# Performance work log

Hardware: AMD Instinct MI355X
Metric: run time of the kernel (lower is better)

Reference implementation:

```python
import jax, jax.numpy as jnp
import numpy as np

B, N, S, H = 8, 512, 4096, 1024

def setup_inputs() -> dict:
    key = jax.random.key(0)
    k1, k2, k3 = jax.random.split(key, 3)
    doc_state = jax.random.normal(k1, (B, S, H), dtype=jnp.float32)
    # token->node membership mask (soft weights in [0,1), structurally a sparse/binary mask)
    nodes_mapping = jax.random.uniform(k2, (B, N, S), dtype=jnp.float32)
    # node lengths: positive, in [1, S) to avoid divide-by-near-zero
    nodes_len = jax.random.uniform(k3, (B, N), dtype=jnp.float32, minval=1.0, maxval=float(S))
    return {"doc_state": doc_state, "nodes_mapping": nodes_mapping, "nodes_len": nodes_len}

def reference(doc_state, nodes_mapping, nodes_len):
    # Faithful math: sum_s nodes_mapping[b,n,s] * doc_state[b,s,h] / nodes_len[b,n]
    # Expressed as a batched matmul instead of materializing [B,N,S,H].
    pooled = jnp.einsum('bns,bsh->bnh', nodes_mapping, doc_state)
    return pooled / nodes_len[:, :, None]
```

## Files before the change

kernel.cpp:

```cpp
#include <hip/hip_runtime.h>
#include <hip/hip_bf16.h>


typedef __bf16 bf16x8 __attribute__((ext_vector_type(8)));
typedef float  f32x4  __attribute__((ext_vector_type(4)));

#define MFMA16(a, b, c) __builtin_amdgcn_mfma_f32_16x16x32_bf16(a, b, c, 0, 0, 0)

constexpr int Bsz = 8;
constexpr int Nn  = 512;
constexpr int Ss  = 4096;
constexpr int Hh  = 1024;

constexpr int BM = 128, BN = 128, BK = 32;
constexpr int LDK = BK + 8;
constexpr int NT = Ss / BK;

__global__ __launch_bounds__(256, 1)
void mean_pool_gemm(const float* __restrict__ doc,
                    const float* __restrict__ map,
                    const float* __restrict__ len,
                    float* __restrict__ out)
{
    __shared__ __align__(16) __bf16 As[2][BM * LDK];
    __shared__ __align__(16) __bf16 Bs[2][BN * LDK];

    const int blk = blockIdx.x;
    const int b   = blk >> 5;
    const int mt  = (blk >> 3) & 3;
    const int ht  = blk & 7;
    const int n0  = mt * BM;
    const int h0  = ht * BN;

    const int tid  = threadIdx.x;
    const int wave = tid >> 6;
    const int lane = tid & 63;
    const int wr   = wave >> 1;
    const int wc   = wave & 1;
    const int l15  = lane & 15;
    const int l4   = lane >> 4;

    const float* Ab = map + (size_t)b * Nn * Ss + (size_t)n0 * Ss;
    const float* Bb = doc + (size_t)b * Ss * Hh + h0;

    const int ra = tid >> 1;
    const int ka = (tid & 1) * 16;
    const int hb  = tid & 127;
    const int kb0 = tid >> 7;

    f32x4 aR[4];
    float bR[2][8];
    f32x4 acc[4][4] = {};

    {
        const float* ap = Ab + (size_t)ra * Ss + ka;
        #pragma unroll
        for (int i = 0; i < 4; i++) aR[i] = *(const f32x4*)(ap + i * 4);
        #pragma unroll
        for (int tt = 0; tt < 2; tt++) {
            const float* bp = Bb + (size_t)((kb0 + tt * 2) * 8) * Hh + hb;
            #pragma unroll
            for (int j = 0; j < 8; j++) bR[tt][j] = bp[(size_t)j * Hh];
        }
        bf16x8 v0, v1;
        #pragma unroll
        for (int i = 0; i < 8; i++) {
            v0[i] = (__bf16)aR[i >> 2][i & 3];
            v1[i] = (__bf16)aR[2 + (i >> 2)][i & 3];
        }
        *(bf16x8*)&As[0][ra * LDK + ka]     = v0;
        *(bf16x8*)&As[0][ra * LDK + ka + 8] = v1;
        #pragma unroll
        for (int tt = 0; tt < 2; tt++) {
            bf16x8 w;
            #pragma unroll
            for (int j = 0; j < 8; j++) w[j] = (__bf16)bR[tt][j];
            *(bf16x8*)&Bs[0][hb * LDK + (kb0 + tt * 2) * 8] = w;
        }
    }
    __syncthreads();

    int cur = 0;
    for (int t = 0; t < NT; ++t) {
        if (t + 1 < NT) {
            const int s0 = (t + 1) * BK;
            const float* ap = Ab + (size_t)ra * Ss + s0 + ka;
            #pragma unroll
            for (int i = 0; i < 4; i++) aR[i] = *(const f32x4*)(ap + i * 4);
            #pragma unroll
            for (int tt = 0; tt < 2; tt++) {
                const float* bp = Bb + (size_t)(s0 + (kb0 + tt * 2) * 8) * Hh + hb;
                #pragma unroll
                for (int j = 0; j < 8; j++) bR[tt][j] = bp[(size_t)j * Hh];
            }
        }

        {
            bf16x8 aF[4], bF[4];
            #pragma unroll
            for (int m = 0; m < 4; m++)
                aF[m] = *(const bf16x8*)&As[cur][(wr * 64 + m * 16 + l15) * LDK + l4 * 8];
            #pragma unroll
            for (int n = 0; n < 4; n++)
                bF[n] = *(const bf16x8*)&Bs[cur][(wc * 64 + n * 16 + l15) * LDK + l4 * 8];
            #pragma unroll
            for (int m = 0; m < 4; m++)
                #pragma unroll
                for (int n = 0; n < 4; n++)
                    acc[m][n] = MFMA16(aF[m], bF[n], acc[m][n]);
        }

        if (t + 1 < NT) {
            __syncthreads();
            bf16x8 v0, v1;
            #pragma unroll
            for (int i = 0; i < 8; i++) {
                v0[i] = (__bf16)aR[i >> 2][i & 3];
                v1[i] = (__bf16)aR[2 + (i >> 2)][i & 3];
            }
            *(bf16x8*)&As[cur ^ 1][ra * LDK + ka]     = v0;
            *(bf16x8*)&As[cur ^ 1][ra * LDK + ka + 8] = v1;
            #pragma unroll
            for (int tt = 0; tt < 2; tt++) {
                bf16x8 w;
                #pragma unroll
                for (int j = 0; j < 8; j++) w[j] = (__bf16)bR[tt][j];
                *(bf16x8*)&Bs[cur ^ 1][hb * LDK + (kb0 + tt * 2) * 8] = w;
            }
            __syncthreads();
            cur ^= 1;
        }
    }

    const float* lenb = len + b * Nn + n0 + wr * 64;
    float* ob = out + (size_t)b * Nn * Hh + (size_t)(n0 + wr * 64) * Hh + h0 + wc * 64;
    #pragma unroll
    for (int m = 0; m < 4; m++) {
        float inv[4];
        #pragma unroll
        for (int j = 0; j < 4; j++) inv[j] = 1.0f / lenb[m * 16 + l4 * 4 + j];
        #pragma unroll
        for (int n = 0; n < 4; n++) {
            #pragma unroll
            for (int j = 0; j < 4; j++) {
                const int row = m * 16 + l4 * 4 + j;
                ob[(size_t)row * Hh + n * 16 + l15] = acc[m][n][j] * inv[j];
            }
        }
    }
}

extern "C" void kernel_launch(void* const* d_in, const int* in_sizes, int n_in,
                              void* d_out, int out_size, void* d_ws, size_t ws_size,
                              hipStream_t stream) {
    const float* doc = (const float*)d_in[0];
    const float* map = (const float*)d_in[1];
    const float* len = (const float*)d_in[2];
    float* out = (float*)d_out;

    dim3 grid(Bsz * (Nn / BM) * (Hh / BN));
    dim3 block(256);
    hipLaunchKernelGGL(mean_pool_gemm, grid, block, 0, stream, doc, map, len, out);
}
```

Measured before the change: 322.2 us.

## Shrink GEMM tiles to 64x64 and remap blocks so each batch stays on one XCD

Tiles shrink from 128x128 to 64x64, which raises the grid from 256 to 1024 workgroups and allows up to four per CU so the MI355X's compute units are fully occupied. The block index is also permuted so that consecutive hardware-dispatched blocks, which go round-robin across the 8 XCDs, map to the same batch on one XCD. This is meant to improve L2 reuse of the fp32 operands. The cost is less data reuse per tile, so each workgroup loads more global memory and issues fewer MFMAs per shared-memory load.

```diff
diff --git a/kernel.cpp b/kernel.cpp
--- a/kernel.cpp
+++ b/kernel.cpp
@@ -12,11 +12,12 @@
 constexpr int Ss  = 4096;
 constexpr int Hh  = 1024;
 
-constexpr int BM = 128, BN = 128, BK = 32;
+constexpr int BM = 64, BN = 64, BK = 32;
 constexpr int LDK = BK + 8;
 constexpr int NT = Ss / BK;
+constexpr int NWG = Bsz * (Nn / BM) * (Hh / BN);
 
-__global__ __launch_bounds__(256, 1)
+__global__ __launch_bounds__(256, 4)
 void mean_pool_gemm(const float* __restrict__ doc,
                     const float* __restrict__ map,
                     const float* __restrict__ len,
@@ -25,10 +26,12 @@
     __shared__ __align__(16) __bf16 As[2][BM * LDK];
     __shared__ __align__(16) __bf16 Bs[2][BN * LDK];
 
-    const int blk = blockIdx.x;
-    const int b   = blk >> 5;
-    const int mt  = (blk >> 3) & 3;
-    const int ht  = blk & 7;
+    const int blk = (blockIdx.x & 7) * (NWG / 8) + (blockIdx.x >> 3);
+
+    const int b   = blk >> 7;
+    const int rem = blk & 127;
+    const int mt  = rem >> 4;
+    const int ht  = rem & 15;
     const int n0  = mt * BM;
     const int h0  = ht * BN;
 
@@ -43,40 +46,31 @@
     const float* Ab = map + (size_t)b * Nn * Ss + (size_t)n0 * Ss;
     const float* Bb = doc + (size_t)b * Ss * Hh + h0;
 
-    const int ra = tid >> 1;
-    const int ka = (tid & 1) * 16;
-    const int hb  = tid & 127;
-    const int kb0 = tid >> 7;
+    const int ra = tid >> 2;
+    const int ka = (tid & 3) * 8;
+    const int hbb = tid & 63;
+    const int kb  = tid >> 6;
 
-    f32x4 aR[4];
-    float bR[2][8];
-    f32x4 acc[4][4] = {};
+    f32x4 aR[2];
+    float bR[8];
+    f32x4 acc[2][2] = {};
 
     {
         const float* ap = Ab + (size_t)ra * Ss + ka;
+        aR[0] = *(const f32x4*)(ap);
+        aR[1] = *(const f32x4*)(ap + 4);
+        const float* bp = Bb + (size_t)(kb * 8) * Hh + hbb;
         #pragma unroll
-        for (int i = 0; i < 4; i++) aR[i] = *(const f32x4*)(ap + i * 4);
-        #pragma unroll
-        for (int tt = 0; tt < 2; tt++) {
-            const float* bp = Bb + (size_t)((kb0 + tt * 2) * 8) * Hh + hb;
-            #pragma unroll
-            for (int j = 0; j < 8; j++) bR[tt][j] = bp[(size_t)j * Hh];
-        }
-        bf16x8 v0, v1;
+        for (int j = 0; j < 8; j++) bR[j] = bp[(size_t)j * Hh];
+
+        bf16x8 va, vb;
         #pragma unroll
         for (int i = 0; i < 8; i++) {
-            v0[i] = (__bf16)aR[i >> 2][i & 3];
-            v1[i] = (__bf16)aR[2 + (i >> 2)][i & 3];
+            va[i] = (__bf16)aR[i >> 2][i & 3];
+            vb[i] = (__bf16)bR[i];
         }
-        *(bf16x8*)&As[0][ra * LDK + ka]     = v0;
-        *(bf16x8*)&As[0][ra * LDK + ka + 8] = v1;
-        #pragma unroll
-        for (int tt = 0; tt < 2; tt++) {
-            bf16x8 w;
-            #pragma unroll
-            for (int j = 0; j < 8; j++) w[j] = (__bf16)bR[tt][j];
-            *(bf16x8*)&Bs[0][hb * LDK + (kb0 + tt * 2) * 8] = w;
-        }
+        *(bf16x8*)&As[0][ra * LDK + ka]      = va;
+        *(bf16x8*)&Bs[0][hbb * LDK + kb * 8] = vb;
     }
     __syncthreads();
 
@@ -85,62 +79,52 @@
         if (t + 1 < NT) {
             const int s0 = (t + 1) * BK;
             const float* ap = Ab + (size_t)ra * Ss + s0 + ka;
+            aR[0] = *(const f32x4*)(ap);
+            aR[1] = *(const f32x4*)(ap + 4);
+            const float* bp = Bb + (size_t)(s0 + kb * 8) * Hh + hbb;
             #pragma unroll
-            for (int i = 0; i < 4; i++) aR[i] = *(const f32x4*)(ap + i * 4);
-            #pragma unroll
-            for (int tt = 0; tt < 2; tt++) {
-                const float* bp = Bb + (size_t)(s0 + (kb0 + tt * 2) * 8) * Hh + hb;
-                #pragma unroll
-                for (int j = 0; j < 8; j++) bR[tt][j] = bp[(size_t)j * Hh];
-            }
+            for (int j = 0; j < 8; j++) bR[j] = bp[(size_t)j * Hh];
         }
 
         {
-            bf16x8 aF[4], bF[4];
+            bf16x8 aF[2], bF[2];
             #pragma unroll
-            for (int m = 0; m < 4; m++)
-                aF[m] = *(const bf16x8*)&As[cur][(wr * 64 + m * 16 + l15) * LDK + l4 * 8];
+            for (int m = 0; m < 2; m++)
+                aF[m] = *(const bf16x8*)&As[cur][(wr * 32 + m * 16 + l15) * LDK + l4 * 8];
             #pragma unroll
-            for (int n = 0; n < 4; n++)
-                bF[n] = *(const bf16x8*)&Bs[cur][(wc * 64 + n * 16 + l15) * LDK + l4 * 8];
+            for (int n = 0; n < 2; n++)
+                bF[n] = *(const bf16x8*)&Bs[cur][(wc * 32 + n * 16 + l15) * LDK + l4 * 8];
             #pragma unroll
-            for (int m = 0; m < 4; m++)
+            for (int m = 0; m < 2; m++)
                 #pragma unroll
-                for (int n = 0; n < 4; n++)
+                for (int n = 0; n < 2; n++)
                     acc[m][n] = MFMA16(aF[m], bF[n], acc[m][n]);
         }
 
         if (t + 1 < NT) {
             __syncthreads();
-            bf16x8 v0, v1;
+            bf16x8 va, vb;
             #pragma unroll
             for (int i = 0; i < 8; i++) {
-                v0[i] = (__bf16)aR[i >> 2][i & 3];
-                v1[i] = (__bf16)aR[2 + (i >> 2)][i & 3];
+                va[i] = (__bf16)aR[i >> 2][i & 3];
+                vb[i] = (__bf16)bR[i];
             }
-            *(bf16x8*)&As[cur ^ 1][ra * LDK + ka]     = v0;
-            *(bf16x8*)&As[cur ^ 1][ra * LDK + ka + 8] = v1;
-            #pragma unroll
-            for (int tt = 0; tt < 2; tt++) {
-                bf16x8 w;
-                #pragma unroll
-                for (int j = 0; j < 8; j++) w[j] = (__bf16)bR[tt][j];
-                *(bf16x8*)&Bs[cur ^ 1][hb * LDK + (kb0 + tt * 2) * 8] = w;
-            }
+            *(bf16x8*)&As[cur ^ 1][ra * LDK + ka]      = va;
+            *(bf16x8*)&Bs[cur ^ 1][hbb * LDK + kb * 8] = vb;
             __syncthreads();
             cur ^= 1;
         }
     }
 
-    const float* lenb = len + b * Nn + n0 + wr * 64;
-    float* ob = out + (size_t)b * Nn * Hh + (size_t)(n0 + wr * 64) * Hh + h0 + wc * 64;
+    const float* lenb = len + b * Nn + n0 + wr * 32;
+    float* ob = out + (size_t)b * Nn * Hh + (size_t)(n0 + wr * 32) * Hh + h0 + wc * 32;
     #pragma unroll
-    for (int m = 0; m < 4; m++) {
+    for (int m = 0; m < 2; m++) {
         float inv[4];
         #pragma unroll
         for (int j = 0; j < 4; j++) inv[j] = 1.0f / lenb[m * 16 + l4 * 4 + j];
         #pragma unroll
-        for (int n = 0; n < 4; n++) {
+        for (int n = 0; n < 2; n++) {
             #pragma unroll
             for (int j = 0; j < 4; j++) {
                 const int row = m * 16 + l4 * 4 + j;
@@ -158,7 +142,7 @@
     const float* len = (const float*)d_in[2];
     float* out = (float*)d_out;
 
-    dim3 grid(Bsz * (Nn / BM) * (Hh / BN));
+    dim3 grid(NWG);
     dim3 block(256);
     hipLaunchKernelGGL(mean_pool_gemm, grid, block, 0, stream, doc, map, len, out);
 }
```

Measured after the change: 316.9 us. About the same (-1.6%).
